# Optimization experiments

Measured on AMD Instinct MI355X. Metric: run time of the kernel, lower is better.

Reference implementation:

```python
import jax, jax.numpy as jnp
import numpy as np

HEADS = 16  # init_kwargs['heads']


def setup_inputs() -> dict:
    key = jax.random.key(0)
    k1, k2, k3, k4, k5, k6 = jax.random.split(key, 6)
    N, L, E = 2, 2048, 1024
    return {
        "values": jax.random.normal(k1, (N, L, E), dtype=jnp.float32),
        "key": jax.random.normal(k2, (N, L, E), dtype=jnp.float32),
        "query": jax.random.normal(k3, (N, L, E), dtype=jnp.float32),
        "mask": jax.random.randint(k4, (N, 1, L, L), 0, 2, dtype=jnp.int32),
        # fc_out: Linear(heads*head_dim=E, E) with bias
        "W_out": jax.random.normal(k5, (E, E), dtype=jnp.float32) / np.sqrt(E),
        "b_out": jax.random.normal(k6, (E,), dtype=jnp.float32) * 0.01,
    }


def reference(values, key, query, mask, W_out, b_out):
    N, Lq, E = query.shape
    Lk = key.shape[1]
    H = HEADS
    D = E // H  # head_dim = 64
    q = query.reshape(N, Lq, H, D)
    k = key.reshape(N, Lk, H, D)
    v = values.reshape(N, Lk, H, D)
    # energy: (N, H, Q, K)
    energy = jnp.einsum("nqhd,nkhd->nhqk", q, k)
    # masked_fill BEFORE scaling, as in the original
    energy = jnp.where(mask == 0, jnp.float32(-1e20), energy)
    attn = jax.nn.softmax(energy / np.float32(np.sqrt(D)), axis=3)
    out = jnp.einsum("nhqk,nkhd->nqhd", attn, v).reshape(N, Lq, H * D)
    return out @ W_out.T + b_out
```

## Files before the change

### kernel.cpp

```cpp
#include <hip/hip_runtime.h>

#define L_SEQ  2048
#define EMB    1024
#define NHEAD  16
#define HDIM   64
#define NBATCH 2

typedef unsigned short u16;
typedef unsigned int   u32;
typedef unsigned long long u64;
typedef short bf16x8 __attribute__((ext_vector_type(8)));
typedef float f32x4  __attribute__((ext_vector_type(4)));
typedef int   i32x4  __attribute__((ext_vector_type(4)));

static __device__ __forceinline__ u16 f2bf(float x) {
    union { float f; unsigned u; } a; a.f = x;
    unsigned r = a.u + 0x7FFFu + ((a.u >> 16) & 1u);
    return (u16)(r >> 16);
}
static __device__ __forceinline__ void cvt8(const float4& a, const float4& b, u16* o, float s) {
    o[0]=f2bf(a.x*s); o[1]=f2bf(a.y*s); o[2]=f2bf(a.z*s); o[3]=f2bf(a.w*s);
    o[4]=f2bf(b.x*s); o[5]=f2bf(b.y*s); o[6]=f2bf(b.z*s); o[7]=f2bf(b.w*s);
}

static __device__ __forceinline__ u32 cvt_pk_bf16(float lo, float hi) {
    u32 r;
    asm("v_cvt_pk_bf16_f32 %0, %1, %2" : "=v"(r) : "v"(lo), "v"(hi));
    return r;
}
static __device__ __forceinline__ void permswap32(u32 &x, u32 &y) {
    asm("v_permlane32_swap_b32 %0, %1" : "+v"(x), "+v"(y));
}
static __device__ __forceinline__ void permswap16(u32 &x, u32 &y) {
    asm("v_permlane16_swap_b32 %0, %1" : "+v"(x), "+v"(y));
}

__global__ void pack_mask(const int* __restrict__ Mg, u64* __restrict__ maskp)
{
    const int wave = threadIdx.x >> 6;
    const int lane = threadIdx.x & 63;
    const int row  = blockIdx.x * 4 + wave;
    const int* mp = Mg + (size_t)row * L_SEQ + lane;
    u64* op = maskp + (size_t)row * (L_SEQ / 64);
    for (int t = 0; t < L_SEQ / 64; ++t) {
        u64 b = __ballot(mp[t * 64] != 0);
        if (lane == 0) op[t] = b;
    }
}

__global__ __launch_bounds__(256)
void prep_qkv(const float* __restrict__ Qg, const float* __restrict__ Kg,
              const float* __restrict__ Vg, u16* __restrict__ Qb,
              u16* __restrict__ Kb, u16* __restrict__ Vt)
{
    const int t = blockIdx.x, h = blockIdx.y, n = blockIdx.z;
    const int tid = threadIdx.x;
    const int row = tid >> 2;
    const int dc  = (tid & 3) * 16;

    __shared__ u16 Vl2[64][72];

    const size_t gin = ((size_t)(n * L_SEQ) + t * 64 + row) * EMB + h * HDIM + dc;

    {
        const float qs = 0.125f * 1.44269504f;
        u16 o[16];
        cvt8(*(const float4*)(Qg + gin),     *(const float4*)(Qg + gin + 4),  o,     qs);
        cvt8(*(const float4*)(Qg + gin + 8), *(const float4*)(Qg + gin + 12), o + 8, qs);
        *(uint4*)(Qb + gin)     = *(const uint4*)o;
        *(uint4*)(Qb + gin + 8) = *(const uint4*)&o[8];
    }
    {
        u16 o[16];
        cvt8(*(const float4*)(Kg + gin),     *(const float4*)(Kg + gin + 4),  o,     1.f);
        cvt8(*(const float4*)(Kg + gin + 8), *(const float4*)(Kg + gin + 12), o + 8, 1.f);
        size_t ko = ((size_t)(n * NHEAD + h) * L_SEQ + t * 64 + row) * HDIM + dc;
        *(uint4*)(Kb + ko)     = *(const uint4*)o;
        *(uint4*)(Kb + ko + 8) = *(const uint4*)&o[8];
    }
    {
        u16 o[16];
        cvt8(*(const float4*)(Vg + gin),     *(const float4*)(Vg + gin + 4),  o,     1.f);
        cvt8(*(const float4*)(Vg + gin + 8), *(const float4*)(Vg + gin + 12), o + 8, 1.f);
        #pragma unroll
        for (int j = 0; j < 16; ++j) Vl2[dc + j][row] = o[j];
    }
    __syncthreads();
    {
        const int d  = tid >> 2;
        const int kc = (tid & 3) * 16;
        size_t vo = ((size_t)(n * NHEAD + h) * HDIM + d) * L_SEQ + t * 64 + kc;
        *(uint4*)(Vt + vo)     = *(const uint4*)&Vl2[d][kc];
        *(uint4*)(Vt + vo + 8) = *(const uint4*)&Vl2[d][kc + 8];
    }
}

__global__ void wcvt(const float* __restrict__ W, u16* __restrict__ Wb)
{
    int i = (blockIdx.x * 256 + threadIdx.x) * 8;
    float4 a = *(const float4*)(W + i);
    float4 b = *(const float4*)(W + i + 4);
    u16 o[8];
    cvt8(a, b, o, 1.f);
    *(uint4*)(Wb + i) = *(const uint4*)o;
}

__global__ __launch_bounds__(256, 2)
void attn_kernel(const u16* __restrict__ Qb, const u16* __restrict__ Kb,
                 const u16* __restrict__ Vt, const u64* __restrict__ maskp,
                 u16* __restrict__ Og)
{
    const int qblk = blockIdx.x;
    const int h    = blockIdx.y;
    const int n    = blockIdx.z;
    const int tid  = threadIdx.x;
    const int wave = tid >> 6;
    const int lane = tid & 63;
    const int l16  = lane & 15;
    const int quad = lane >> 4;

    __shared__ u16 Kl[64][72];
    __shared__ u16 Vl[64][72];

    const int q0 = qblk * 128 + wave * 32;

    bf16x8 qf[2][2];
    #pragma unroll
    for (int qs = 0; qs < 2; ++qs) {
        const u16* qp = Qb + ((size_t)(n * L_SEQ) + q0 + qs * 16 + l16) * EMB + h * HDIM;
        qf[qs][0] = *(const bf16x8*)(qp + quad * 8);
        qf[qs][1] = *(const bf16x8*)(qp + 32 + quad * 8);
    }

    f32x4 acc[2][4];
    #pragma unroll
    for (int qs = 0; qs < 2; ++qs)
        #pragma unroll
        for (int c = 0; c < 4; ++c)
            #pragma unroll
            for (int r = 0; r < 4; ++r) acc[qs][c][r] = 0.f;
    float lsum[2] = {0.f, 0.f};

    const u16* kbase = Kb + (size_t)(n * NHEAD + h) * L_SEQ * HDIM;
    const u16* vbase = Vt + (size_t)(n * NHEAD + h) * HDIM * L_SEQ;
    const u64* mbase = maskp + ((size_t)(n * L_SEQ) + q0 + l16) * (L_SEQ / 64);
    const int  mqs   = 16 * (L_SEQ / 64);

    const int srow = tid >> 2;
    const int scol = (tid & 3) * 16;

    uint4 kr0, kr1, vr0, vr1;
    u64 mr[2];

    {
        const u16* kp = kbase + (size_t)srow * HDIM + scol;
        const u16* vp = vbase + (size_t)srow * L_SEQ + scol;
        kr0 = *(const uint4*)kp;  kr1 = *(const uint4*)(kp + 8);
        vr0 = *(const uint4*)vp;  vr1 = *(const uint4*)(vp + 8);
        mr[0] = mbase[0];
        mr[1] = mbase[mqs];
    }

    for (int t = 0; t < L_SEQ / 64; ++t) {
        __syncthreads();
        *(uint4*)&Kl[srow][scol]     = kr0;
        *(uint4*)&Kl[srow][scol + 8] = kr1;
        *(uint4*)&Vl[srow][scol]     = vr0;
        *(uint4*)&Vl[srow][scol + 8] = vr1;
        u64 mcur0 = mr[0], mcur1 = mr[1];

        if (t + 1 < L_SEQ / 64) {
            const u16* kp = kbase + (size_t)((t + 1) * 64 + srow) * HDIM + scol;
            const u16* vp = vbase + (size_t)srow * L_SEQ + (t + 1) * 64 + scol;
            kr0 = *(const uint4*)kp;  kr1 = *(const uint4*)(kp + 8);
            vr0 = *(const uint4*)vp;  vr1 = *(const uint4*)(vp + 8);
            mr[0] = mbase[t + 1];
            mr[1] = mbase[mqs + t + 1];
        }
        __syncthreads();

        const int sh = quad * 4;
        u32 mlo[2], mhi[2];
        mlo[0] = (u32)mcur0 >> sh;  mhi[0] = (u32)(mcur0 >> 32) >> sh;
        mlo[1] = (u32)mcur1 >> sh;  mhi[1] = (u32)(mcur1 >> 32) >> sh;

        u32 Dw[2][8];
        #pragma unroll
        for (int cc = 0; cc < 4; ++cc) {
            bf16x8 k0 = *(const bf16x8*)&Kl[cc * 16 + l16][quad * 8];
            bf16x8 k1 = *(const bf16x8*)&Kl[cc * 16 + l16][32 + quad * 8];
            f32x4 z0; z0[0]=0.f; z0[1]=0.f; z0[2]=0.f; z0[3]=0.f;
            f32x4 z1 = z0;
            z0 = __builtin_amdgcn_mfma_f32_16x16x32_bf16(k0, qf[0][0], z0, 0, 0, 0);
            z0 = __builtin_amdgcn_mfma_f32_16x16x32_bf16(k1, qf[0][1], z0, 0, 0, 0);
            z1 = __builtin_amdgcn_mfma_f32_16x16x32_bf16(k0, qf[1][0], z1, 0, 0, 0);
            z1 = __builtin_amdgcn_mfma_f32_16x16x32_bf16(k1, qf[1][1], z1, 0, 0, 0);

            #pragma unroll
            for (int qs = 0; qs < 2; ++qs) {
                const f32x4& z = (qs == 0) ? z0 : z1;
                u32 w = (cc < 2) ? mlo[qs] : mhi[qs];
                float pv[4];
                #pragma unroll
                for (int r = 0; r < 4; ++r) {
                    const int pos = (cc & 1) * 16 + r;
                    int sm = (int)(w << (31 - pos)) >> 31;
                    float p = __builtin_amdgcn_exp2f(z[r]);
                    p = __int_as_float(__float_as_int(p) & sm);
                    lsum[qs] += p;
                    pv[r] = p;
                }
                Dw[qs][2 * cc]     = cvt_pk_bf16(pv[0], pv[1]);
                Dw[qs][2 * cc + 1] = cvt_pk_bf16(pv[2], pv[3]);
            }
        }

        #pragma unroll
        for (int kc = 0; kc < 2; ++kc) {
            bf16x8 pf[2];
            #pragma unroll
            for (int qs = 0; qs < 2; ++qs) {
                u32 b0 = Dw[qs][4 * kc + 0], b2 = Dw[qs][4 * kc + 2];
                permswap32(b0, b2); permswap16(b0, b2);
                u32 b1 = Dw[qs][4 * kc + 1], b3 = Dw[qs][4 * kc + 3];
                permswap32(b1, b3); permswap16(b1, b3);
                union { i32x4 i; bf16x8 v; } pu;
                pu.i[0] = (int)b0; pu.i[1] = (int)b1; pu.i[2] = (int)b2; pu.i[3] = (int)b3;
                pf[qs] = pu.v;
            }
            #pragma unroll
            for (int dc = 0; dc < 4; ++dc) {
                bf16x8 vf = *(const bf16x8*)&Vl[dc * 16 + l16][kc * 32 + quad * 8];
                acc[0][dc] = __builtin_amdgcn_mfma_f32_16x16x32_bf16(vf, pf[0], acc[0][dc], 0, 0, 0);
                acc[1][dc] = __builtin_amdgcn_mfma_f32_16x16x32_bf16(vf, pf[1], acc[1][dc], 0, 0, 0);
            }
        }
    }

    #pragma unroll
    for (int qs = 0; qs < 2; ++qs) {
        float s = lsum[qs];
        s += __shfl_xor(s, 16);
        s += __shfl_xor(s, 32);
        float inv = 1.f / s;

        u16* op = Og + ((size_t)(n * L_SEQ) + q0 + qs * 16 + l16) * EMB + h * HDIM + quad * 4;
        #pragma unroll
        for (int dc = 0; dc < 4; ++dc) {
            u32 u0 = cvt_pk_bf16(acc[qs][dc][0] * inv, acc[qs][dc][1] * inv);
            u32 u1 = cvt_pk_bf16(acc[qs][dc][2] * inv, acc[qs][dc][3] * inv);
            uint2 st; st.x = u0; st.y = u1;
            *(uint2*)(op + dc * 16) = st;
        }
    }
}

__global__ __launch_bounds__(256, 4)
void out_gemm(const u16* __restrict__ A, const u16* __restrict__ B,
              const float* __restrict__ bias, float* __restrict__ out)
{
    const int bn  = blockIdx.x;
    const int bm  = blockIdx.y;
    const int tid = threadIdx.x;
    const int wave = tid >> 6;
    const int lane = tid & 63;
    const int l16  = lane & 15;
    const int quad = lane >> 4;
    const int wr = wave >> 1, wc = wave & 1;

    __shared__ u16 Al[64][72];
    __shared__ u16 Bl[64][72];

    f32x4 acc[2][2];
    #pragma unroll
    for (int i = 0; i < 2; ++i)
        #pragma unroll
        for (int j = 0; j < 2; ++j)
            #pragma unroll
            for (int r = 0; r < 4; ++r) acc[i][j][r] = 0.f;

    const int srow = tid >> 2;
    const int kc   = (tid & 3) * 16;

    const u16* ap = A + (size_t)(bm * 64 + srow) * EMB + kc;
    const u16* bp = B + (size_t)(bn * 64 + srow) * EMB + kc;

    uint4 ar0 = *(const uint4*)ap,        ar1 = *(const uint4*)(ap + 8);
    uint4 br0 = *(const uint4*)bp,        br1 = *(const uint4*)(bp + 8);

    for (int k0 = 0; k0 < EMB; k0 += 64) {
        __syncthreads();
        *(uint4*)&Al[srow][kc]     = ar0;
        *(uint4*)&Al[srow][kc + 8] = ar1;
        *(uint4*)&Bl[srow][kc]     = br0;
        *(uint4*)&Bl[srow][kc + 8] = br1;
        if (k0 + 64 < EMB) {
            ar0 = *(const uint4*)(ap + k0 + 64);  ar1 = *(const uint4*)(ap + k0 + 72);
            br0 = *(const uint4*)(bp + k0 + 64);  br1 = *(const uint4*)(bp + k0 + 72);
        }
        __syncthreads();

        #pragma unroll
        for (int kk = 0; kk < 2; ++kk) {
            bf16x8 af[2], bfr[2];
            #pragma unroll
            for (int i = 0; i < 2; ++i)
                af[i] = *(const bf16x8*)&Al[wr * 32 + i * 16 + l16][kk * 32 + quad * 8];
            #pragma unroll
            for (int j = 0; j < 2; ++j)
                bfr[j] = *(const bf16x8*)&Bl[wc * 32 + j * 16 + l16][kk * 32 + quad * 8];
            #pragma unroll
            for (int i = 0; i < 2; ++i)
                #pragma unroll
                for (int j = 0; j < 2; ++j)
                    acc[i][j] = __builtin_amdgcn_mfma_f32_16x16x32_bf16(af[i], bfr[j], acc[i][j], 0, 0, 0);
        }
    }

    #pragma unroll
    for (int j = 0; j < 2; ++j) {
        int col = bn * 64 + wc * 32 + j * 16 + l16;
        float bv = bias[col];
        #pragma unroll
        for (int i = 0; i < 2; ++i) {
            int row0 = bm * 64 + wr * 32 + i * 16 + quad * 4;
            #pragma unroll
            for (int r = 0; r < 4; ++r)
                out[(size_t)(row0 + r) * EMB + col] = acc[i][j][r] + bv;
        }
    }
}

extern "C" void kernel_launch(void* const* d_in, const int* in_sizes, int n_in,
                              void* d_out, int out_size, void* d_ws, size_t ws_size,
                              hipStream_t stream)
{
    const float* Vg = (const float*)d_in[0];
    const float* Kg = (const float*)d_in[1];
    const float* Qg = (const float*)d_in[2];
    const int*   Mg = (const int*)d_in[3];
    const float* Wg = (const float*)d_in[4];
    const float* Bg = (const float*)d_in[5];
    float* Og = (float*)d_out;

    const size_t QKV = (size_t)NBATCH * L_SEQ * EMB;
    char* ws = (char*)d_ws;
    u16* attn_ws = (u16*)ws;
    u16* Wb      = (u16*)(ws + QKV * 2);
    u16* Qb      = (u16*)(ws + QKV * 2 + 2 * 1024 * 1024);
    u16* Kb      = Qb + QKV;
    u16* Vt      = Kb + QKV;
    u64* maskp   = (u64*)(Vt + QKV);

    pack_mask<<<dim3(NBATCH * L_SEQ / 4), 256, 0, stream>>>(Mg, maskp);
    prep_qkv<<<dim3(L_SEQ / 64, NHEAD, NBATCH), 256, 0, stream>>>(Qg, Kg, Vg, Qb, Kb, Vt);
    wcvt<<<dim3(EMB * EMB / (256 * 8)), 256, 0, stream>>>(Wg, Wb);

    dim3 g1(L_SEQ / 128, NHEAD, NBATCH);
    attn_kernel<<<g1, 256, 0, stream>>>(Qb, Kb, Vt, maskp, attn_ws);

    dim3 g2(EMB / 64, (NBATCH * L_SEQ) / 64);
    out_gemm<<<g2, 256, 0, stream>>>(attn_ws, Wb, Bg, Og);
}
```

Before: 220.4 us.

## Software-pipeline attention loop with multi-buffered LDS and fuse prep kernels

Merges the mask packing, QKV conversion and weight conversion kernels into one launch that dispatches work by block index. The attention loop now double-buffers K and quad-buffers V in shared memory, prefetches two tiles ahead, and runs the P·V MFMAs for the previous tile while computing QK scores for the current one. This cuts the loop to one barrier per iteration. Row sums are split into four partial accumulators to shorten dependency chains. The cost is more LDS per block (about 55 KB), which may limit occupancy, plus higher register pressure.

Result: faster. 204.4 us (-7.3%).

```diff
diff --git a/kernel.cpp b/kernel.cpp
--- a/kernel.cpp
+++ b/kernel.cpp
@@ -5,6 +5,7 @@
 #define NHEAD  16
 #define HDIM   64
 #define NBATCH 2
+#define NT     (L_SEQ / 64)
 
 typedef unsigned short u16;
 typedef unsigned int   u32;
@@ -35,74 +36,164 @@
     asm("v_permlane16_swap_b32 %0, %1" : "+v"(x), "+v"(y));
 }
 
-__global__ void pack_mask(const int* __restrict__ Mg, u64* __restrict__ maskp)
-{
-    const int wave = threadIdx.x >> 6;
-    const int lane = threadIdx.x & 63;
-    const int row  = blockIdx.x * 4 + wave;
-    const int* mp = Mg + (size_t)row * L_SEQ + lane;
-    u64* op = maskp + (size_t)row * (L_SEQ / 64);
-    for (int t = 0; t < L_SEQ / 64; ++t) {
-        u64 b = __ballot(mp[t * 64] != 0);
-        if (lane == 0) op[t] = b;
-    }
-}
-
 __global__ __launch_bounds__(256)
-void prep_qkv(const float* __restrict__ Qg, const float* __restrict__ Kg,
-              const float* __restrict__ Vg, u16* __restrict__ Qb,
-              u16* __restrict__ Kb, u16* __restrict__ Vt)
-{
-    const int t = blockIdx.x, h = blockIdx.y, n = blockIdx.z;
+void prep_fused(const float* __restrict__ Qg, const float* __restrict__ Kg,
+                const float* __restrict__ Vg, const int* __restrict__ Mg,
+                const float* __restrict__ Wg,
+                u16* __restrict__ Qb, u16* __restrict__ Kb, u16* __restrict__ Vt,
+                u64* __restrict__ maskp, u16* __restrict__ Wb)
+{
+    const int bid = blockIdx.x;
     const int tid = threadIdx.x;
-    const int row = tid >> 2;
-    const int dc  = (tid & 3) * 16;
-
     __shared__ u16 Vl2[64][72];
 
-    const size_t gin = ((size_t)(n * L_SEQ) + t * 64 + row) * EMB + h * HDIM + dc;
-
-    {
-        const float qs = 0.125f * 1.44269504f;
-        u16 o[16];
-        cvt8(*(const float4*)(Qg + gin),     *(const float4*)(Qg + gin + 4),  o,     qs);
-        cvt8(*(const float4*)(Qg + gin + 8), *(const float4*)(Qg + gin + 12), o + 8, qs);
-        *(uint4*)(Qb + gin)     = *(const uint4*)o;
-        *(uint4*)(Qb + gin + 8) = *(const uint4*)&o[8];
-    }
-    {
-        u16 o[16];
-        cvt8(*(const float4*)(Kg + gin),     *(const float4*)(Kg + gin + 4),  o,     1.f);
-        cvt8(*(const float4*)(Kg + gin + 8), *(const float4*)(Kg + gin + 12), o + 8, 1.f);
-        size_t ko = ((size_t)(n * NHEAD + h) * L_SEQ + t * 64 + row) * HDIM + dc;
-        *(uint4*)(Kb + ko)     = *(const uint4*)o;
-        *(uint4*)(Kb + ko + 8) = *(const uint4*)&o[8];
-    }
-    {
-        u16 o[16];
-        cvt8(*(const float4*)(Vg + gin),     *(const float4*)(Vg + gin + 4),  o,     1.f);
-        cvt8(*(const float4*)(Vg + gin + 8), *(const float4*)(Vg + gin + 12), o + 8, 1.f);
-        #pragma unroll
-        for (int j = 0; j < 16; ++j) Vl2[dc + j][row] = o[j];
-    }
+    if (bid < 1024) {
+        const int wave = tid >> 6;
+        const int lane = tid & 63;
+        const int row  = bid * 4 + wave;
+        const int* mp = Mg + (size_t)row * L_SEQ + lane;
+        u64* op = maskp + (size_t)row * NT;
+        for (int tt = 0; tt < NT; ++tt) {
+            u64 b = __ballot(mp[tt * 64] != 0);
+            if (lane == 0) op[tt] = b;
+        }
+    } else if (bid < 2048) {
+        const int b  = bid - 1024;
+        const int tt = b & 31, hh = (b >> 5) & 15, nn = b >> 9;
+        const int row = tid >> 2;
+        const int dc  = (tid & 3) * 16;
+
+        const size_t gin = ((size_t)(nn * L_SEQ) + tt * 64 + row) * EMB + hh * HDIM + dc;
+
+        {
+            const float qs = 0.125f * 1.44269504f;
+            u16 o[16];
+            cvt8(*(const float4*)(Qg + gin),     *(const float4*)(Qg + gin + 4),  o,     qs);
+            cvt8(*(const float4*)(Qg + gin + 8), *(const float4*)(Qg + gin + 12), o + 8, qs);
+            *(uint4*)(Qb + gin)     = *(const uint4*)o;
+            *(uint4*)(Qb + gin + 8) = *(const uint4*)&o[8];
+        }
+        {
+            u16 o[16];
+            cvt8(*(const float4*)(Kg + gin),     *(const float4*)(Kg + gin + 4),  o,     1.f);
+            cvt8(*(const float4*)(Kg + gin + 8), *(const float4*)(Kg + gin + 12), o + 8, 1.f);
+            size_t ko = ((size_t)(nn * NHEAD + hh) * L_SEQ + tt * 64 + row) * HDIM + dc;
+            *(uint4*)(Kb + ko)     = *(const uint4*)o;
+            *(uint4*)(Kb + ko + 8) = *(const uint4*)&o[8];
+        }
+        {
+            u16 o[16];
+            cvt8(*(const float4*)(Vg + gin),     *(const float4*)(Vg + gin + 4),  o,     1.f);
+            cvt8(*(const float4*)(Vg + gin + 8), *(const float4*)(Vg + gin + 12), o + 8, 1.f);
+            #pragma unroll
+            for (int j = 0; j < 16; ++j) Vl2[dc + j][row] = o[j];
+        }
+        __syncthreads();
+        {
+            const int d  = tid >> 2;
+            const int kc = (tid & 3) * 16;
+            size_t vo = ((size_t)(nn * NHEAD + hh) * HDIM + d) * L_SEQ + tt * 64 + kc;
+            *(uint4*)(Vt + vo)     = *(const uint4*)&Vl2[d][kc];
+            *(uint4*)(Vt + vo + 8) = *(const uint4*)&Vl2[d][kc + 8];
+        }
+    } else {
+        int i = ((bid - 2048) * 256 + tid) * 8;
+        float4 a = *(const float4*)(Wg + i);
+        float4 b4 = *(const float4*)(Wg + i + 4);
+        u16 o[8];
+        cvt8(a, b4, o, 1.f);
+        *(uint4*)(Wb + i) = *(const uint4*)o;
+    }
+}
+
+static __device__ __forceinline__ void pv_step(
+    const u32 (&Dwp)[2][8], const u16 (&Vb)[64][72],
+    f32x4 (&acc)[2][4], int l16, int quad)
+{
+    #pragma unroll
+    for (int kc = 0; kc < 2; ++kc) {
+        bf16x8 pf[2];
+        #pragma unroll
+        for (int qs = 0; qs < 2; ++qs) {
+            u32 b0 = Dwp[qs][4 * kc + 0], b2 = Dwp[qs][4 * kc + 2];
+            permswap32(b0, b2); permswap16(b0, b2);
+            u32 b1 = Dwp[qs][4 * kc + 1], b3 = Dwp[qs][4 * kc + 3];
+            permswap32(b1, b3); permswap16(b1, b3);
+            union { i32x4 i; bf16x8 v; } pu;
+            pu.i[0] = (int)b0; pu.i[1] = (int)b1; pu.i[2] = (int)b2; pu.i[3] = (int)b3;
+            pf[qs] = pu.v;
+        }
+        #pragma unroll
+        for (int dc = 0; dc < 4; ++dc) {
+            bf16x8 vf = *(const bf16x8*)&Vb[dc * 16 + l16][kc * 32 + quad * 8];
+            acc[0][dc] = __builtin_amdgcn_mfma_f32_16x16x32_bf16(vf, pf[0], acc[0][dc], 0, 0, 0);
+            acc[1][dc] = __builtin_amdgcn_mfma_f32_16x16x32_bf16(vf, pf[1], acc[1][dc], 0, 0, 0);
+        }
+    }
+}
+
+static __device__ __forceinline__ void attn_tile(
+    int t, int kbuf, int vprev, int kw, int vw,
+    u32 (&Dwc)[2][8], u32 (&Dwp)[2][8],
+    u16 (&Kl)[2][64][72], u16 (&Vl)[4][64][72],
+    const bf16x8 (&qf)[2][2], f32x4 (&acc)[2][4], float (&ls)[2][4],
+    uint4& kr0, uint4& kr1, uint4& vr0, uint4& vr1,
+    u64& mr0, u64& mr1,
+    const u16* kbase, const u16* vbase, const u64* mbase, int mqs,
+    int srow, int scol, int l16, int quad)
+{
+    if (t < NT - 1) {
+        *(uint4*)&Kl[kw][srow][scol]     = kr0;
+        *(uint4*)&Kl[kw][srow][scol + 8] = kr1;
+        *(uint4*)&Vl[vw][srow][scol]     = vr0;
+        *(uint4*)&Vl[vw][srow][scol + 8] = vr1;
+    }
+    u64 mcur0 = mr0, mcur1 = mr1;
+    if (t < NT - 1) { mr0 = mbase[t + 1]; mr1 = mbase[mqs + t + 1]; }
+    if (t < NT - 2) {
+        const u16* kp = kbase + (size_t)((t + 2) * 64 + srow) * HDIM + scol;
+        const u16* vp = vbase + (size_t)srow * L_SEQ + (t + 2) * 64 + scol;
+        kr0 = *(const uint4*)kp;  kr1 = *(const uint4*)(kp + 8);
+        vr0 = *(const uint4*)vp;  vr1 = *(const uint4*)(vp + 8);
+    }
+
+    const int sh = quad * 4;
+    u32 mlo0 = (u32)mcur0 >> sh, mhi0 = (u32)(mcur0 >> 32) >> sh;
+    u32 mlo1 = (u32)mcur1 >> sh, mhi1 = (u32)(mcur1 >> 32) >> sh;
+    #pragma unroll
+    for (int cc = 0; cc < 4; ++cc) {
+        bf16x8 k0 = *(const bf16x8*)&Kl[kbuf][cc * 16 + l16][quad * 8];
+        bf16x8 k1 = *(const bf16x8*)&Kl[kbuf][cc * 16 + l16][32 + quad * 8];
+        f32x4 z0; z0[0]=0.f; z0[1]=0.f; z0[2]=0.f; z0[3]=0.f;
+        f32x4 z1 = z0;
+        z0 = __builtin_amdgcn_mfma_f32_16x16x32_bf16(k0, qf[0][0], z0, 0, 0, 0);
+        z0 = __builtin_amdgcn_mfma_f32_16x16x32_bf16(k1, qf[0][1], z0, 0, 0, 0);
+        z1 = __builtin_amdgcn_mfma_f32_16x16x32_bf16(k0, qf[1][0], z1, 0, 0, 0);
+        z1 = __builtin_amdgcn_mfma_f32_16x16x32_bf16(k1, qf[1][1], z1, 0, 0, 0);
+
+        #pragma unroll
+        for (int qs = 0; qs < 2; ++qs) {
+            const f32x4& z = (qs == 0) ? z0 : z1;
+            u32 w = (cc < 2) ? ((qs == 0) ? mlo0 : mlo1)
+                             : ((qs == 0) ? mhi0 : mhi1);
+            float pv[4];
+            #pragma unroll
+            for (int r = 0; r < 4; ++r) {
+                const int pos = (cc & 1) * 16 + r;
+                int sm = (int)(w << (31 - pos)) >> 31;
+                float p = __builtin_amdgcn_exp2f(z[r]);
+                p = __int_as_float(__float_as_int(p) & sm);
+                ls[qs][r] += p;
+                pv[r] = p;
+            }
+            Dwc[qs][2 * cc]     = cvt_pk_bf16(pv[0], pv[1]);
+            Dwc[qs][2 * cc + 1] = cvt_pk_bf16(pv[2], pv[3]);
+        }
+    }
+
+    pv_step(Dwp, Vl[vprev], acc, l16, quad);
+
     __syncthreads();
-    {
-        const int d  = tid >> 2;
-        const int kc = (tid & 3) * 16;
-        size_t vo = ((size_t)(n * NHEAD + h) * HDIM + d) * L_SEQ + t * 64 + kc;
-        *(uint4*)(Vt + vo)     = *(const uint4*)&Vl2[d][kc];
-        *(uint4*)(Vt + vo + 8) = *(const uint4*)&Vl2[d][kc + 8];
-    }
-}
-
-__global__ void wcvt(const float* __restrict__ W, u16* __restrict__ Wb)
-{
-    int i = (blockIdx.x * 256 + threadIdx.x) * 8;
-    float4 a = *(const float4*)(W + i);
-    float4 b = *(const float4*)(W + i + 4);
-    u16 o[8];
-    cvt8(a, b, o, 1.f);
-    *(uint4*)(Wb + i) = *(const uint4*)o;
 }
 
 __global__ __launch_bounds__(256, 2)
@@ -119,8 +210,8 @@
     const int l16  = lane & 15;
     const int quad = lane >> 4;
 
-    __shared__ u16 Kl[64][72];
-    __shared__ u16 Vl[64][72];
+    __shared__ u16 Kl[2][64][72];
+    __shared__ u16 Vl[4][64][72];
 
     const int q0 = qblk * 128 + wave * 32;
 
@@ -139,107 +230,75 @@
         for (int c = 0; c < 4; ++c)
             #pragma unroll
             for (int r = 0; r < 4; ++r) acc[qs][c][r] = 0.f;
-    float lsum[2] = {0.f, 0.f};
+    float ls[2][4];
+    #pragma unroll
+    for (int qs = 0; qs < 2; ++qs)
+        #pragma unroll
+        for (int r = 0; r < 4; ++r) ls[qs][r] = 0.f;
+
+    u32 DwA[2][8], DwB[2][8];
+    #pragma unroll
+    for (int qs = 0; qs < 2; ++qs)
+        #pragma unroll
+        for (int i = 0; i < 8; ++i) { DwA[qs][i] = 0u; DwB[qs][i] = 0u; }
 
     const u16* kbase = Kb + (size_t)(n * NHEAD + h) * L_SEQ * HDIM;
     const u16* vbase = Vt + (size_t)(n * NHEAD + h) * HDIM * L_SEQ;
-    const u64* mbase = maskp + ((size_t)(n * L_SEQ) + q0 + l16) * (L_SEQ / 64);
-    const int  mqs   = 16 * (L_SEQ / 64);
+    const u64* mbase = maskp + ((size_t)(n * L_SEQ) + q0 + l16) * NT;
+    const int  mqs   = 16 * NT;
 
     const int srow = tid >> 2;
     const int scol = (tid & 3) * 16;
 
     uint4 kr0, kr1, vr0, vr1;
-    u64 mr[2];
+    u64 mr0, mr1;
 
     {
         const u16* kp = kbase + (size_t)srow * HDIM + scol;
         const u16* vp = vbase + (size_t)srow * L_SEQ + scol;
         kr0 = *(const uint4*)kp;  kr1 = *(const uint4*)(kp + 8);
         vr0 = *(const uint4*)vp;  vr1 = *(const uint4*)(vp + 8);
-        mr[0] = mbase[0];
-        mr[1] = mbase[mqs];
-    }
-
-    for (int t = 0; t < L_SEQ / 64; ++t) {
-        __syncthreads();
-        *(uint4*)&Kl[srow][scol]     = kr0;
-        *(uint4*)&Kl[srow][scol + 8] = kr1;
-        *(uint4*)&Vl[srow][scol]     = vr0;
-        *(uint4*)&Vl[srow][scol + 8] = vr1;
-        u64 mcur0 = mr[0], mcur1 = mr[1];
-
-        if (t + 1 < L_SEQ / 64) {
-            const u16* kp = kbase + (size_t)((t + 1) * 64 + srow) * HDIM + scol;
-            const u16* vp = vbase + (size_t)srow * L_SEQ + (t + 1) * 64 + scol;
-            kr0 = *(const uint4*)kp;  kr1 = *(const uint4*)(kp + 8);
-            vr0 = *(const uint4*)vp;  vr1 = *(const uint4*)(vp + 8);
-            mr[0] = mbase[t + 1];
-            mr[1] = mbase[mqs + t + 1];
-        }
-        __syncthreads();
-
-        const int sh = quad * 4;
-        u32 mlo[2], mhi[2];
-        mlo[0] = (u32)mcur0 >> sh;  mhi[0] = (u32)(mcur0 >> 32) >> sh;
-        mlo[1] = (u32)mcur1 >> sh;  mhi[1] = (u32)(mcur1 >> 32) >> sh;
-
-        u32 Dw[2][8];
-        #pragma unroll
-        for (int cc = 0; cc < 4; ++cc) {
-            bf16x8 k0 = *(const bf16x8*)&Kl[cc * 16 + l16][quad * 8];
-            bf16x8 k1 = *(const bf16x8*)&Kl[cc * 16 + l16][32 + quad * 8];
-            f32x4 z0; z0[0]=0.f; z0[1]=0.f; z0[2]=0.f; z0[3]=0.f;
-            f32x4 z1 = z0;
-            z0 = __builtin_amdgcn_mfma_f32_16x16x32_bf16(k0, qf[0][0], z0, 0, 0, 0);
-            z0 = __builtin_amdgcn_mfma_f32_16x16x32_bf16(k1, qf[0][1], z0, 0, 0, 0);
-            z1 = __builtin_amdgcn_mfma_f32_16x16x32_bf16(k0, qf[1][0], z1, 0, 0, 0);
-            z1 = __builtin_amdgcn_mfma_f32_16x16x32_bf16(k1, qf[1][1], z1, 0, 0, 0);
-
-            #pragma unroll
-            for (int qs = 0; qs < 2; ++qs) {
-                const f32x4& z = (qs == 0) ? z0 : z1;
-                u32 w = (cc < 2) ? mlo[qs] : mhi[qs];
-                float pv[4];
-                #pragma unroll
-                for (int r = 0; r < 4; ++r) {
-                    const int pos = (cc & 1) * 16 + r;
-                    int sm = (int)(w << (31 - pos)) >> 31;
-                    float p = __builtin_amdgcn_exp2f(z[r]);
-                    p = __int_as_float(__float_as_int(p) & sm);
-                    lsum[qs] += p;
-                    pv[r] = p;
-                }
-                Dw[qs][2 * cc]     = cvt_pk_bf16(pv[0], pv[1]);
-                Dw[qs][2 * cc + 1] = cvt_pk_bf16(pv[2], pv[3]);
-            }
-        }
-
-        #pragma unroll
-        for (int kc = 0; kc < 2; ++kc) {
-            bf16x8 pf[2];
-            #pragma unroll
-            for (int qs = 0; qs < 2; ++qs) {
-                u32 b0 = Dw[qs][4 * kc + 0], b2 = Dw[qs][4 * kc + 2];
-                permswap32(b0, b2); permswap16(b0, b2);
-                u32 b1 = Dw[qs][4 * kc + 1], b3 = Dw[qs][4 * kc + 3];
-                permswap32(b1, b3); permswap16(b1, b3);
-                union { i32x4 i; bf16x8 v; } pu;
-                pu.i[0] = (int)b0; pu.i[1] = (int)b1; pu.i[2] = (int)b2; pu.i[3] = (int)b3;
-                pf[qs] = pu.v;
-            }
-            #pragma unroll
-            for (int dc = 0; dc < 4; ++dc) {
-                bf16x8 vf = *(const bf16x8*)&Vl[dc * 16 + l16][kc * 32 + quad * 8];
-                acc[0][dc] = __builtin_amdgcn_mfma_f32_16x16x32_bf16(vf, pf[0], acc[0][dc], 0, 0, 0);
-                acc[1][dc] = __builtin_amdgcn_mfma_f32_16x16x32_bf16(vf, pf[1], acc[1][dc], 0, 0, 0);
-            }
-        }
-    }
+    }
+    *(uint4*)&Kl[0][srow][scol]     = kr0;
+    *(uint4*)&Kl[0][srow][scol + 8] = kr1;
+    *(uint4*)&Vl[0][srow][scol]     = vr0;
+    *(uint4*)&Vl[0][srow][scol + 8] = vr1;
+    {
+        u32* vz = (u32*)&Vl[3][0][0];
+        #pragma unroll
+        for (int i = 0; i < 9; ++i) vz[tid + i * 256] = 0u;
+    }
+    {
+        const u16* kp = kbase + (size_t)(64 + srow) * HDIM + scol;
+        const u16* vp = vbase + (size_t)srow * L_SEQ + 64 + scol;
+        kr0 = *(const uint4*)kp;  kr1 = *(const uint4*)(kp + 8);
+        vr0 = *(const uint4*)vp;  vr1 = *(const uint4*)(vp + 8);
+    }
+    mr0 = mbase[0];
+    mr1 = mbase[mqs];
+    __syncthreads();
+
+    for (int j = 0; j < 8; ++j) {
+        const int t = j * 4;
+        attn_tile(t + 0, 0, 3, 1, 1, DwA, DwB, Kl, Vl, qf, acc, ls,
+                  kr0, kr1, vr0, vr1, mr0, mr1, kbase, vbase, mbase, mqs,
+                  srow, scol, l16, quad);
+        attn_tile(t + 1, 1, 0, 0, 2, DwB, DwA, Kl, Vl, qf, acc, ls,
+                  kr0, kr1, vr0, vr1, mr0, mr1, kbase, vbase, mbase, mqs,
+                  srow, scol, l16, quad);
+        attn_tile(t + 2, 0, 1, 1, 3, DwA, DwB, Kl, Vl, qf, acc, ls,
+                  kr0, kr1, vr0, vr1, mr0, mr1, kbase, vbase, mbase, mqs,
+                  srow, scol, l16, quad);
+        attn_tile(t + 3, 1, 2, 0, 0, DwB, DwA, Kl, Vl, qf, acc, ls,
+                  kr0, kr1, vr0, vr1, mr0, mr1, kbase, vbase, mbase, mqs,
+                  srow, scol, l16, quad);
+    }
+
+    pv_step(DwB, Vl[3], acc, l16, quad);
 
     #pragma unroll
     for (int qs = 0; qs < 2; ++qs) {
-        float s = lsum[qs];
+        float s = (ls[qs][0] + ls[qs][1]) + (ls[qs][2] + ls[qs][3]);
         s += __shfl_xor(s, 16);
         s += __shfl_xor(s, 32);
         float inv = 1.f / s;
@@ -352,9 +411,8 @@
     u16* Vt      = Kb + QKV;
     u64* maskp   = (u64*)(Vt + QKV);
 
-    pack_mask<<<dim3(NBATCH * L_SEQ / 4), 256, 0, stream>>>(Mg, maskp);
-    prep_qkv<<<dim3(L_SEQ / 64, NHEAD, NBATCH), 256, 0, stream>>>(Qg, Kg, Vg, Qb, Kb, Vt);
-    wcvt<<<dim3(EMB * EMB / (256 * 8)), 256, 0, stream>>>(Wg, Wb);
+    prep_fused<<<dim3(2560), 256, 0, stream>>>(Qg, Kg, Vg, Mg, Wg,
+                                               Qb, Kb, Vt, maskp, Wb);
 
     dim3 g1(L_SEQ / 128, NHEAD, NBATCH);
     attn_kernel<<<g1, 256, 0, stream>>>(Qb, Kb, Vt, maskp, attn_ws);
```
